# Optimization experiments

Measured on AMD Instinct MI355X. Metric: run time of the kernel, lower is better.

## Reference

```python
import jax, jax.numpy as jnp
import numpy as np

B, T, C = 2, 2048, 2048
N, K, H = 16, 4, 128      # heads, kv heads, head dim
G = N // K                # query groups per kv head
ROPE_THETA = 10000.0
N_LAYERS = 24
SOFTCAP = 50.0


def _sine_table(features, length, max_timescale):
    fraction = jnp.arange(0, features, 2, dtype=jnp.float32) / features
    timescale = max_timescale ** fraction  # min_timescale = 1.0
    sinusoid = jnp.einsum('i,j->ij', jnp.arange(length, dtype=jnp.float32),
                          1.0 / timescale, precision=jax.lax.Precision.HIGHEST)
    sinusoid = jnp.concatenate([sinusoid, sinusoid], axis=-1)  # (length, features)
    return jnp.sin(sinusoid), jnp.cos(sinusoid)


def _rotate_half(x):
    x1, x2 = jnp.split(x, 2, axis=-1)
    return jnp.concatenate([-x2, x1], axis=-1)


def setup_inputs() -> dict:
    key = jax.random.key(0)
    kx, kq, kk, kv, ko = jax.random.split(key, 5)
    init_std = np.sqrt(2.0 / (5.0 * C)).astype(np.float32)
    wang_std = np.float32(2.0 / N_LAYERS / np.sqrt(N * H))
    return {
        'x': jax.random.normal(kx, (B, T, C), dtype=jnp.float32),
        'q_kernel': jax.random.normal(kq, (C, N * H), dtype=jnp.float32) * init_std,
        'k_kernel': jax.random.normal(kk, (C, K * H), dtype=jnp.float32) * init_std,
        'v_kernel': jax.random.normal(kv, (C, K * H), dtype=jnp.float32) * init_std,
        'out_kernel': jax.random.normal(ko, (N * H, C), dtype=jnp.float32) * wang_std,
    }


def reference(x, q_kernel, k_kernel, v_kernel, out_kernel):
    q = jnp.dot(x, q_kernel).reshape(B, T, K, G, H)
    k = jnp.dot(x, k_kernel).reshape(B, T, K, H)
    v = jnp.dot(x, v_kernel).reshape(B, T, K, H)

    # RoPE (note original passes cos into the `sin` slot and vice versa by name,
    # but the computation uses cos with identity part and sin with rotate_half).
    sin, cos = _sine_table(H, T, ROPE_THETA)
    qcos = cos[None, :, None, None, :]  # (1,T,1,1,H)
    qsin = sin[None, :, None, None, :]
    kcos = cos[None, :, None, :]        # (1,T,1,H)
    ksin = sin[None, :, None, :]
    q = q * qcos + _rotate_half(q) * qsin
    k = k * kcos + _rotate_half(k) * ksin

    scale = jax.lax.rsqrt(jnp.float32(H))
    logits = jnp.einsum('btkgh,bskh->bkgts', q * scale, k)  # (B,K,G,T,S)
    logits = jnp.tanh(logits / SOFTCAP) * SOFTCAP
    causal = jnp.tril(jnp.ones((T, T), dtype=jnp.bool_))
    neg = jnp.asarray(-0.7 * jnp.finfo(logits.dtype).max, dtype=logits.dtype)
    logits = jnp.where(causal[None, None, None, :, :], logits, neg)
    probs = jax.nn.softmax(logits.astype(jnp.float32), axis=-1).astype(logits.dtype)
    encoded = jnp.einsum('bkgts,bskh->btkgh', probs, v)
    encoded = encoded.reshape(B, T, N * H)
    return jnp.dot(encoded, out_kernel)
```

## Files before the change

### kernel.cpp

```cpp
#include <hip/hip_runtime.h>
#include <stdint.h>

typedef unsigned short u16;
typedef __bf16 bf16x8 __attribute__((ext_vector_type(8)));
typedef __bf16 bf16x4 __attribute__((ext_vector_type(4)));
typedef float f32x4 __attribute__((ext_vector_type(4)));

#define T_SEQ 2048
#define KVH 4

__device__ __forceinline__ u16 f2b(float f) {
  uint32_t u = __builtin_bit_cast(uint32_t, f);
  u += 0x7FFFu + ((u >> 16) & 1u);
  return (u16)(u >> 16);
}
__device__ __forceinline__ float b2f(u16 h) {
  uint32_t u = ((uint32_t)h) << 16;
  return __builtin_bit_cast(float, u);
}

__device__ __forceinline__ void gload16(const void* g, void* l) {
  __builtin_amdgcn_global_load_lds((const __attribute__((address_space(1))) void*)g,
                                   (__attribute__((address_space(3))) void*)l, 16, 0, 0);
}

__global__ void k_f32_to_bf16(const float* __restrict__ in, u16* __restrict__ out, int n4) {
  int i = blockIdx.x * blockDim.x + threadIdx.x;
  if (i >= n4) return;
  float4 v = reinterpret_cast<const float4*>(in)[i];
  ushort4 o;
  o.x = f2b(v.x); o.y = f2b(v.y); o.z = f2b(v.z); o.w = f2b(v.w);
  reinterpret_cast<ushort4*>(out)[i] = o;
}

__global__ void k_transpose_f32_bf16(const float* __restrict__ in, u16* __restrict__ out,
                                     int R, int Cc) {
  __shared__ float tile[32][33];
  const int c0 = blockIdx.x * 32, r0 = blockIdx.y * 32;
  const int tx = threadIdx.x, ty = threadIdx.y;
  for (int i = ty; i < 32; i += 8) tile[i][tx] = in[(size_t)(r0 + i) * Cc + c0 + tx];
  __syncthreads();
  for (int i = ty; i < 32; i += 8) out[(size_t)(c0 + i) * R + r0 + tx] = f2b(tile[tx][i]);
}

template <int OUT_BF16>
__global__ __launch_bounds__(256, 3) void k_gemm(const u16* __restrict__ A,
                                                 const u16* __restrict__ Bt,
                                                 void* __restrict__ Cp,
                                                 int M, int N, int Kd,
                                                 int lda, int ldb, int ldc) {
  __align__(16) __shared__ u16 As[128 * 32];
  __align__(16) __shared__ u16 Bs[128 * 32];
  const int tid = threadIdx.x;
  const int wid = tid >> 6, lane = tid & 63;
  const int lg = lane >> 4, lm = lane & 15;
  const int bm = blockIdx.x, bn = blockIdx.y;
  const int wr = wid >> 1, wc = wid & 1;

  const int srow = wid * 32 + (lane >> 2);
  const int scol = (lane & 3) * 8;
  const u16* ap0 = A + (size_t)(bm * 128 + srow) * lda + scol;
  const u16* ap1 = ap0 + (size_t)16 * lda;
  const u16* bp0 = Bt + (size_t)(bn * 128 + srow) * ldb + scol;
  const u16* bp1 = bp0 + (size_t)16 * ldb;
  u16* asDst0 = As + wid * 1024;
  u16* asDst1 = As + wid * 1024 + 512;
  u16* bsDst0 = Bs + wid * 1024;
  u16* bsDst1 = Bs + wid * 1024 + 512;

  const f32x4 z4 = {0.f, 0.f, 0.f, 0.f};
  f32x4 acc[4][4];
#pragma unroll
  for (int i = 0; i < 4; ++i)
#pragma unroll
    for (int j = 0; j < 4; ++j) acc[i][j] = z4;

  const int nk = Kd >> 5;
  for (int kb = 0; kb < nk; ++kb) {
    gload16(ap0, asDst0);
    gload16(ap1, asDst1);
    gload16(bp0, bsDst0);
    gload16(bp1, bsDst1);
    ap0 += 32; ap1 += 32; bp0 += 32; bp1 += 32;
    __syncthreads();
    bf16x8 af[4], bfr[4];
#pragma unroll
    for (int i = 0; i < 4; ++i)
      af[i] = *(const bf16x8*)(As + (wr * 64 + i * 16 + lm) * 32 + lg * 8);
#pragma unroll
    for (int j = 0; j < 4; ++j)
      bfr[j] = *(const bf16x8*)(Bs + (wc * 64 + j * 16 + lm) * 32 + lg * 8);
#pragma unroll
    for (int i = 0; i < 4; ++i)
#pragma unroll
      for (int j = 0; j < 4; ++j)
        acc[i][j] = __builtin_amdgcn_mfma_f32_16x16x32_bf16(af[i], bfr[j], acc[i][j], 0, 0, 0);
    __syncthreads();
  }

#pragma unroll
  for (int i = 0; i < 4; ++i) {
    const int row = bm * 128 + wr * 64 + i * 16 + lg * 4;
#pragma unroll
    for (int j = 0; j < 4; ++j) {
      const int col = bn * 128 + wc * 64 + j * 16 + lm;
#pragma unroll
      for (int r = 0; r < 4; ++r) {
        const float v = acc[i][j][r];
        if (OUT_BF16)
          ((u16*)Cp)[(size_t)(row + r) * ldc + col] = __builtin_bit_cast(u16, (__bf16)v);
        else
          ((float*)Cp)[(size_t)(row + r) * ldc + col] = v;
      }
    }
  }
}

__global__ void k_rope_k(const u16* __restrict__ qkv, u16* __restrict__ kbf) {
  const int idx = blockIdx.x * 256 + threadIdx.x;
  const int j = idx & 63;
  const int kh = (idx >> 6) & 3;
  const int m = idx >> 8;
  const int t = m & (T_SEQ - 1);
  const int b = m >> 11;
  const float inv = __expf((float)j * -0.14391157f);
  const float ang = (float)t * inv;
  float s, c;
  __sincosf(ang, &s, &c);
  const u16* row = qkv + (size_t)m * 3072 + 2048 + kh * 128;
  const float x1 = b2f(row[j]), x2 = b2f(row[j + 64]);
  u16* orow = kbf + ((size_t)(b * KVH + kh) * T_SEQ + t) * 128;
  orow[j] = f2b(x1 * c - x2 * s);
  orow[j + 64] = f2b(x2 * c + x1 * s);
}

__global__ void k_v_transpose(const u16* __restrict__ qkv, u16* __restrict__ vt) {
  __shared__ u16 tile[32][33];
  const int t0 = blockIdx.x * 32, h0 = blockIdx.y * 32, bk = blockIdx.z;
  const int b = bk >> 2, kh = bk & 3;
  const int tx = threadIdx.x, ty = threadIdx.y;
  for (int i = ty; i < 32; i += 8)
    tile[i][tx] = qkv[(size_t)(b * T_SEQ + t0 + i) * 3072 + 2560 + kh * 128 + h0 + tx];
  __syncthreads();
  for (int i = ty; i < 32; i += 8)
    vt[(size_t)bk * (128 * T_SEQ) + (size_t)(h0 + i) * T_SEQ + t0 + tx] = tile[tx][i];
}

__global__ __launch_bounds__(256, 2) void k_attn(const u16* __restrict__ qkv,
                                                 const u16* __restrict__ kbf,
                                                 const u16* __restrict__ vt,
                                                 u16* __restrict__ enc) {
  __shared__ __align__(16) u16 smem[36864];
  u16* const Ks0 = smem;
  u16* const Vs0 = smem + 16384;

  const int n = blockIdx.y, b = blockIdx.z;
  const int qt = (b == 0) ? (15 - blockIdx.x) : blockIdx.x;
  const int kh = n >> 2;
  const int tid = threadIdx.x;
  const int wid = tid >> 6;
  const int lane = tid & 63;
  const int lg = lane >> 4;
  const int lm = lane & 15;
  const int q0w = qt * 128 + wid * 32;
  u16* const Pl = smem + 32768 + wid * 1024;

  bf16x8 qfA[4], qfB[4];
  {
    const u16* qa = qkv + (size_t)(b * T_SEQ + q0w + lm) * 3072 + n * 128 + lg * 8;
    const u16* qb_ = qa + 16 * 3072;
    bf16x8 ra[4], rb[4];
#pragma unroll
    for (int c = 0; c < 4; ++c) {
      ra[c] = *(const bf16x8*)(qa + c * 32);
      rb[c] = *(const bf16x8*)(qb_ + c * 32);
    }
    const float scale = 0.08838834764831845f;
    const float tA = (float)(q0w + lm), tB = (float)(q0w + 16 + lm);
#pragma unroll
    for (int c = 0; c < 2; ++c) {
#pragma unroll
      for (int k = 0; k < 8; ++k) {
        const float inv = __expf((float)(c * 32 + lg * 8 + k) * -0.14391157f);
        float sA, cA, sB, cB;
        __sincosf(tA * inv, &sA, &cA);
        __sincosf(tB * inv, &sB, &cB);
        const float a1 = (float)ra[c][k], a2 = (float)ra[c + 2][k];
        const float b1 = (float)rb[c][k], b2 = (float)rb[c + 2][k];
        qfA[c][k]     = (__bf16)((a1 * cA - a2 * sA) * scale);
        qfA[c + 2][k] = (__bf16)((a2 * cA + a1 * sA) * scale);
        qfB[c][k]     = (__bf16)((b1 * cB - b2 * sB) * scale);
        qfB[c + 2][k] = (__bf16)((b2 * cB + b1 * sB) * scale);
      }
    }
  }
  const u16* const kg = kbf + (size_t)(b * KVH + kh) * T_SEQ * 128;
  const u16* const vg = vt + (size_t)(b * KVH + kh) * 128 * T_SEQ;

  const int swz = lm & 7;
  int koff[4], voff[2], poff[4];
#pragma unroll
  for (int c = 0; c < 4; ++c) koff[c] = lm * 128 + (((c * 4 + lg) ^ swz) * 8);
#pragma unroll
  for (int ks = 0; ks < 2; ++ks) voff[ks] = lm * 64 + (((ks * 4 + lg) ^ swz) * 8);
#pragma unroll
  for (int st = 0; st < 4; ++st)
    poff[st] = lm * 64 + (((st * 2 + (lg >> 1)) ^ swz) * 8) + (lg & 1) * 4;

  const f32x4 z4 = {0.f, 0.f, 0.f, 0.f};
  f32x4 accA[8], accB[8];
#pragma unroll
  for (int h = 0; h < 8; ++h) { accA[h] = z4; accB[h] = z4; }
  float lA = 0.f, lB = 0.f;

  const int ntiles = 2 * qt + 2;

  auto STAGE = [&](int buf, int kb2) {
    const int kv2 = kb2 * 64;
    const u16* ksrc = kg + (size_t)kv2 * 128;
    u16* kdst = Ks0 + buf * 8192;
    u16* vdst = Vs0 + buf * 8192;
#pragma unroll
    for (int i = 0; i < 4; ++i) {
      const int g = tid + i * 256;
      const int row = g >> 4, u = g & 15;
      gload16(ksrc + row * 128 + ((u ^ (row & 7)) * 8), kdst + g * 8);
    }
#pragma unroll
    for (int i = 0; i < 4; ++i) {
      const int g = tid + i * 256;
      const int row = g >> 3, u = g & 7;
      gload16(vg + (size_t)row * T_SEQ + kv2 + ((u ^ (row & 7)) * 8), vdst + g * 8);
    }
  };

  auto tile_pc = [&](f32x4* sa, float* p, float& lsum, int tg, bool needMask, int kv) {
#pragma unroll
    for (int st = 0; st < 4; ++st)
#pragma unroll
      for (int r = 0; r < 4; ++r) p[st * 4 + r] = sa[st][r];
#pragma unroll
    for (int i = 0; i < 16; ++i) {
      const float e = __builtin_amdgcn_exp2f(p[i] * 0.05770780163555853f);
      p[i] = __builtin_amdgcn_exp2f(-144.269504088896f * __builtin_amdgcn_rcpf(e + 1.f));
    }
    if (needMask) {
#pragma unroll
      for (int i = 0; i < 16; ++i) {
        const int sg = kv + (i >> 2) * 16 + lg * 4 + (i & 3);
        if (sg > tg) p[i] = 0.f;
      }
    }
#pragma unroll
    for (int i = 0; i < 16; ++i) lsum += p[i];
  };
  auto tile_pw = [&](const float* p) {
#pragma unroll
    for (int st = 0; st < 4; ++st) {
      bf16x4 w4;
#pragma unroll
      for (int r = 0; r < 4; ++r) w4[r] = (__bf16)p[st * 4 + r];
      *(bf16x4*)(Pl + poff[st]) = w4;
    }
  };

  STAGE(0, 0);
  asm volatile("s_waitcnt vmcnt(0)" ::: "memory");
  __syncthreads();

  for (int kb = 0; kb < ntiles; ++kb) {
    const int cur = kb & 1;
    if (kb + 1 < ntiles) STAGE(cur ^ 1, kb + 1);
    const int kv = kb * 64;
    if (kv <= q0w + 31) {
      const u16* KsC = Ks0 + cur * 8192;
      const u16* VsC = Vs0 + cur * 8192;

      f32x4 saA[4] = {z4, z4, z4, z4};
      f32x4 saB[4] = {z4, z4, z4, z4};
      __builtin_amdgcn_s_setprio(1);
#pragma unroll
      for (int st = 0; st < 4; ++st) {
#pragma unroll
        for (int c = 0; c < 4; ++c) {
          const bf16x8 kf = *(const bf16x8*)(KsC + st * 2048 + koff[c]);
          saA[st] = __builtin_amdgcn_mfma_f32_16x16x32_bf16(kf, qfA[c], saA[st], 0, 0, 0);
          saB[st] = __builtin_amdgcn_mfma_f32_16x16x32_bf16(kf, qfB[c], saB[st], 0, 0, 0);
        }
      }
      __builtin_amdgcn_s_setprio(0);

      float pA[16], pB[16];
      tile_pc(saA, pA, lA, q0w + lm, kv + 63 > q0w, kv);
      tile_pw(pA);
      tile_pc(saB, pB, lB, q0w + 16 + lm, kv + 63 > q0w + 16, kv);
      asm volatile("s_waitcnt lgkmcnt(0)" ::: "memory");
      bf16x8 pfA[2], pfB[2];
#pragma unroll
      for (int ks = 0; ks < 2; ++ks) pfA[ks] = *(const bf16x8*)(Pl + voff[ks]);
      tile_pw(pB);
      asm volatile("s_waitcnt lgkmcnt(0)" ::: "memory");
#pragma unroll
      for (int ks = 0; ks < 2; ++ks) pfB[ks] = *(const bf16x8*)(Pl + voff[ks]);

      __builtin_amdgcn_s_setprio(1);
#pragma unroll
      for (int h = 0; h < 8; ++h) {
#pragma unroll
        for (int ks = 0; ks < 2; ++ks) {
          const bf16x8 vf = *(const bf16x8*)(VsC + h * 1024 + voff[ks]);
          accA[h] = __builtin_amdgcn_mfma_f32_16x16x32_bf16(pfA[ks], vf, accA[h], 0, 0, 0);
          accB[h] = __builtin_amdgcn_mfma_f32_16x16x32_bf16(pfB[ks], vf, accB[h], 0, 0, 0);
        }
      }
      __builtin_amdgcn_s_setprio(0);
    }
    asm volatile("s_waitcnt vmcnt(0)" ::: "memory");
    __syncthreads();
  }

  lA += __shfl_xor(lA, 16); lA += __shfl_xor(lA, 32);
  lB += __shfl_xor(lB, 16); lB += __shfl_xor(lB, 32);
  float liA[4], liB[4];
#pragma unroll
  for (int r = 0; r < 4; ++r) {
    liA[r] = 1.f / __shfl(lA, lg * 4 + r);
    liB[r] = 1.f / __shfl(lB, lg * 4 + r);
  }
#pragma unroll
  for (int h = 0; h < 8; ++h) {
#pragma unroll
    for (int r = 0; r < 4; ++r) {
      const size_t colo = n * 128 + h * 16 + lm;
      enc[(size_t)(b * T_SEQ + q0w + lg * 4 + r) * 2048 + colo] =
          __builtin_bit_cast(u16, (__bf16)(accA[h][r] * liA[r]));
      enc[(size_t)(b * T_SEQ + q0w + 16 + lg * 4 + r) * 2048 + colo] =
          __builtin_bit_cast(u16, (__bf16)(accB[h][r] * liB[r]));
    }
  }
}

extern "C" void kernel_launch(void* const* d_in, const int* in_sizes, int n_in,
                              void* d_out, int out_size, void* d_ws, size_t ws_size,
                              hipStream_t stream) {
  const float* x  = (const float*)d_in[0];
  const float* wq = (const float*)d_in[1];
  const float* wk = (const float*)d_in[2];
  const float* wv = (const float*)d_in[3];
  const float* wo = (const float*)d_in[4];

  char* ws = (char*)d_ws;
  u16* x_bf  = (u16*)(ws);
  u16* wqkvt = (u16*)(ws + 16777216);
  u16* wot   = (u16*)(ws + 29360128);
  u16* qkv   = (u16*)(ws + 37748736);
  u16* enc   = (u16*)(ws + 62914560);
  u16* k_bf  = (u16*)(ws + 79691776);
  u16* vt    = (u16*)(ws + 83886080);
  if (ws_size < 88080384) return;
  (void)in_sizes; (void)n_in; (void)out_size;

  k_f32_to_bf16<<<dim3(8192), dim3(256), 0, stream>>>(x, x_bf, 8388608 / 4);
  k_transpose_f32_bf16<<<dim3(64, 64), dim3(32, 8), 0, stream>>>(wq, wqkvt, 2048, 2048);
  k_transpose_f32_bf16<<<dim3(16, 64), dim3(32, 8), 0, stream>>>(wk, wqkvt + 2048 * 2048, 2048, 512);
  k_transpose_f32_bf16<<<dim3(16, 64), dim3(32, 8), 0, stream>>>(wv, wqkvt + 2560 * 2048, 2048, 512);
  k_transpose_f32_bf16<<<dim3(64, 64), dim3(32, 8), 0, stream>>>(wo, wot, 2048, 2048);
  k_gemm<1><<<dim3(32, 24), dim3(256), 0, stream>>>(x_bf, wqkvt, qkv,
                                                    4096, 3072, 2048, 2048, 2048, 3072);
  k_rope_k<<<dim3(4096), dim3(256), 0, stream>>>(qkv, k_bf);
  k_v_transpose<<<dim3(64, 4, 8), dim3(32, 8), 0, stream>>>(qkv, vt);
  k_attn<<<dim3(16, 16, 2), dim3(256), 0, stream>>>(qkv, k_bf, vt, enc);
  k_gemm<0><<<dim3(32, 16), dim3(256), 0, stream>>>(enc, wot, d_out,
                                                    4096, 2048, 2048, 2048, 2048, 2048);
}
```

Before: 208.8 us.

## Split attention KV range across two warp halves with 4-stage prefetch pipeline

The attention block grows from 256 to 512 threads. Two groups of four waves each process a different 32-key half of every 64-key tile for the same query rows. K/V staging becomes a 4-deep ring buffer with vmcnt-based waits instead of a full drain per tile, and the two halves' partial outputs and row sums are combined through shared memory at the end. This doubles the waves available to hide latency and overlaps loads further ahead, at the cost of double LDS use (one block per CU), a final reduction pass, and narrower MFMA work per wave.

After: 227.2 us. +8.8%, slower.

```diff
diff --git a/kernel.cpp b/kernel.cpp
--- a/kernel.cpp
+++ b/kernel.cpp
@@ -146,24 +146,24 @@
     vt[(size_t)bk * (128 * T_SEQ) + (size_t)(h0 + i) * T_SEQ + t0 + tx] = tile[tx][i];
 }
 
-__global__ __launch_bounds__(256, 2) void k_attn(const u16* __restrict__ qkv,
+__global__ __launch_bounds__(512, 1) void k_attn(const u16* __restrict__ qkv,
                                                  const u16* __restrict__ kbf,
                                                  const u16* __restrict__ vt,
                                                  u16* __restrict__ enc) {
-  __shared__ __align__(16) u16 smem[36864];
-  u16* const Ks0 = smem;
-  u16* const Vs0 = smem + 16384;
+  __shared__ __align__(16) u16 smem[73728];
 
   const int n = blockIdx.y, b = blockIdx.z;
   const int qt = (b == 0) ? (15 - blockIdx.x) : blockIdx.x;
   const int kh = n >> 2;
   const int tid = threadIdx.x;
   const int wid = tid >> 6;
+  const int half = wid >> 2;
+  const int wq = wid & 3;
   const int lane = tid & 63;
   const int lg = lane >> 4;
   const int lm = lane & 15;
-  const int q0w = qt * 128 + wid * 32;
-  u16* const Pl = smem + 32768 + wid * 1024;
+  const int q0w = qt * 128 + wq * 32;
+  u16* const Pl = smem + 65536 + wid * 1024;
 
   bf16x8 qfA[4], qfB[4];
   {
@@ -197,15 +197,14 @@
   const u16* const kg = kbf + (size_t)(b * KVH + kh) * T_SEQ * 128;
   const u16* const vg = vt + (size_t)(b * KVH + kh) * 128 * T_SEQ;
 
-  const int swz = lm & 7;
-  int koff[4], voff[2], poff[4];
-#pragma unroll
-  for (int c = 0; c < 4; ++c) koff[c] = lm * 128 + (((c * 4 + lg) ^ swz) * 8);
-#pragma unroll
-  for (int ks = 0; ks < 2; ++ks) voff[ks] = lm * 64 + (((ks * 4 + lg) ^ swz) * 8);
-#pragma unroll
-  for (int st = 0; st < 4; ++st)
-    poff[st] = lm * 64 + (((st * 2 + (lg >> 1)) ^ swz) * 8) + (lg & 1) * 4;
+  int koff[4];
+#pragma unroll
+  for (int c = 0; c < 4; ++c) koff[c] = lm * 128 + (((c * 4 + lg) ^ (lm & 7)) * 8);
+  const int voffb = lm * 32 + ((lg ^ (lm & 3)) * 8);
+  int poff[2];
+#pragma unroll
+  for (int st = 0; st < 2; ++st)
+    poff[st] = lm * 32 + (((st * 2 + (lg >> 1)) ^ (lm & 3)) * 8) + (lg & 1) * 4;
 
   const f32x4 z4 = {0.f, 0.f, 0.f, 0.f};
   f32x4 accA[8], accB[8];
@@ -215,48 +214,46 @@
 
   const int ntiles = 2 * qt + 2;
 
-  auto STAGE = [&](int buf, int kb2) {
-    const int kv2 = kb2 * 64;
-    const u16* ksrc = kg + (size_t)kv2 * 128;
-    u16* kdst = Ks0 + buf * 8192;
-    u16* vdst = Vs0 + buf * 8192;
-#pragma unroll
-    for (int i = 0; i < 4; ++i) {
-      const int g = tid + i * 256;
-      const int row = g >> 4, u = g & 15;
-      gload16(ksrc + row * 128 + ((u ^ (row & 7)) * 8), kdst + g * 8);
-    }
-#pragma unroll
-    for (int i = 0; i < 4; ++i) {
-      const int g = tid + i * 256;
-      const int row = g >> 3, u = g & 7;
-      gload16(vg + (size_t)row * T_SEQ + kv2 + ((u ^ (row & 7)) * 8), vdst + g * 8);
+  auto STAGE = [&](int buf, int j2) {
+#pragma unroll
+    for (int hh = 0; hh < 2; ++hh) {
+      const int kv2 = j2 * 64 + hh * 32;
+      {
+        const int row = tid >> 4, u = tid & 15;
+        gload16(kg + (size_t)(kv2 + row) * 128 + ((u ^ (row & 7)) * 8),
+                smem + (buf * 2 + hh) * 4096 + tid * 8);
+      }
+      {
+        const int row = tid >> 2, u = tid & 3;
+        gload16(vg + (size_t)row * T_SEQ + kv2 + ((u ^ (row & 3)) * 8),
+                smem + 32768 + (buf * 2 + hh) * 4096 + tid * 8);
+      }
     }
   };
 
-  auto tile_pc = [&](f32x4* sa, float* p, float& lsum, int tg, bool needMask, int kv) {
-#pragma unroll
-    for (int st = 0; st < 4; ++st)
+  auto tile_pc = [&](f32x4* sa, float* p, float& lsum, int tg, bool needMask, int kvh) {
+#pragma unroll
+    for (int st = 0; st < 2; ++st)
 #pragma unroll
       for (int r = 0; r < 4; ++r) p[st * 4 + r] = sa[st][r];
 #pragma unroll
-    for (int i = 0; i < 16; ++i) {
+    for (int i = 0; i < 8; ++i) {
       const float e = __builtin_amdgcn_exp2f(p[i] * 0.05770780163555853f);
       p[i] = __builtin_amdgcn_exp2f(-144.269504088896f * __builtin_amdgcn_rcpf(e + 1.f));
     }
     if (needMask) {
 #pragma unroll
-      for (int i = 0; i < 16; ++i) {
-        const int sg = kv + (i >> 2) * 16 + lg * 4 + (i & 3);
+      for (int i = 0; i < 8; ++i) {
+        const int sg = kvh + (i >> 2) * 16 + lg * 4 + (i & 3);
         if (sg > tg) p[i] = 0.f;
       }
     }
 #pragma unroll
-    for (int i = 0; i < 16; ++i) lsum += p[i];
+    for (int i = 0; i < 8; ++i) lsum += p[i];
   };
   auto tile_pw = [&](const float* p) {
 #pragma unroll
-    for (int st = 0; st < 4; ++st) {
+    for (int st = 0; st < 2; ++st) {
       bf16x4 w4;
 #pragma unroll
       for (int r = 0; r < 4; ++r) w4[r] = (__bf16)p[st * 4 + r];
@@ -264,78 +261,113 @@
     }
   };
 
+  auto COMPUTE = [&](int j) {
+    const int kvh = j * 64 + half * 32;
+    if (kvh > q0w + 31) return;
+    const u16* KsC = smem + ((j & 3) * 2 + half) * 4096;
+    const u16* VsC = smem + 32768 + ((j & 3) * 2 + half) * 4096;
+
+    f32x4 saA[2] = {z4, z4}, saB[2] = {z4, z4};
+    __builtin_amdgcn_s_setprio(1);
+#pragma unroll
+    for (int st = 0; st < 2; ++st) {
+#pragma unroll
+      for (int c = 0; c < 4; ++c) {
+        const bf16x8 kf = *(const bf16x8*)(KsC + st * 2048 + koff[c]);
+        saA[st] = __builtin_amdgcn_mfma_f32_16x16x32_bf16(kf, qfA[c], saA[st], 0, 0, 0);
+        saB[st] = __builtin_amdgcn_mfma_f32_16x16x32_bf16(kf, qfB[c], saB[st], 0, 0, 0);
+      }
+    }
+    __builtin_amdgcn_s_setprio(0);
+
+    float pA[8], pB[8];
+    tile_pc(saA, pA, lA, q0w + lm, kvh + 31 > q0w, kvh);
+    tile_pw(pA);
+    tile_pc(saB, pB, lB, q0w + 16 + lm, kvh + 31 > q0w + 16, kvh);
+    asm volatile("s_waitcnt lgkmcnt(0)" ::: "memory");
+    const bf16x8 pfA = *(const bf16x8*)(Pl + voffb);
+    tile_pw(pB);
+    asm volatile("s_waitcnt lgkmcnt(0)" ::: "memory");
+    const bf16x8 pfB = *(const bf16x8*)(Pl + voffb);
+
+    __builtin_amdgcn_s_setprio(1);
+#pragma unroll
+    for (int h = 0; h < 8; ++h) {
+      const bf16x8 vf = *(const bf16x8*)(VsC + h * 512 + voffb);
+      accA[h] = __builtin_amdgcn_mfma_f32_16x16x32_bf16(pfA, vf, accA[h], 0, 0, 0);
+      accB[h] = __builtin_amdgcn_mfma_f32_16x16x32_bf16(pfB, vf, accB[h], 0, 0, 0);
+    }
+    __builtin_amdgcn_s_setprio(0);
+  };
+
   STAGE(0, 0);
-  asm volatile("s_waitcnt vmcnt(0)" ::: "memory");
+  STAGE(1, 1);
+  for (int j = 0; j < ntiles - 2; ++j) {
+    STAGE((j + 2) & 3, j + 2);
+    asm volatile("s_waitcnt vmcnt(8)" ::: "memory");
+    __builtin_amdgcn_s_barrier();
+    __builtin_amdgcn_sched_barrier(0);
+    COMPUTE(j);
+  }
+  {
+    asm volatile("s_waitcnt vmcnt(4)" ::: "memory");
+    __builtin_amdgcn_s_barrier();
+    __builtin_amdgcn_sched_barrier(0);
+    COMPUTE(ntiles - 2);
+  }
+  {
+    asm volatile("s_waitcnt vmcnt(0)" ::: "memory");
+    __builtin_amdgcn_s_barrier();
+    __builtin_amdgcn_sched_barrier(0);
+    COMPUTE(ntiles - 1);
+  }
+
   __syncthreads();
-
-  for (int kb = 0; kb < ntiles; ++kb) {
-    const int cur = kb & 1;
-    if (kb + 1 < ntiles) STAGE(cur ^ 1, kb + 1);
-    const int kv = kb * 64;
-    if (kv <= q0w + 31) {
-      const u16* KsC = Ks0 + cur * 8192;
-      const u16* VsC = Vs0 + cur * 8192;
-
-      f32x4 saA[4] = {z4, z4, z4, z4};
-      f32x4 saB[4] = {z4, z4, z4, z4};
-      __builtin_amdgcn_s_setprio(1);
-#pragma unroll
-      for (int st = 0; st < 4; ++st) {
-#pragma unroll
-        for (int c = 0; c < 4; ++c) {
-          const bf16x8 kf = *(const bf16x8*)(KsC + st * 2048 + koff[c]);
-          saA[st] = __builtin_amdgcn_mfma_f32_16x16x32_bf16(kf, qfA[c], saA[st], 0, 0, 0);
-          saB[st] = __builtin_amdgcn_mfma_f32_16x16x32_bf16(kf, qfB[c], saB[st], 0, 0, 0);
-        }
-      }
-      __builtin_amdgcn_s_setprio(0);
-
-      float pA[16], pB[16];
-      tile_pc(saA, pA, lA, q0w + lm, kv + 63 > q0w, kv);
-      tile_pw(pA);
-      tile_pc(saB, pB, lB, q0w + 16 + lm, kv + 63 > q0w + 16, kv);
-      asm volatile("s_waitcnt lgkmcnt(0)" ::: "memory");
-      bf16x8 pfA[2], pfB[2];
-#pragma unroll
-      for (int ks = 0; ks < 2; ++ks) pfA[ks] = *(const bf16x8*)(Pl + voff[ks]);
-      tile_pw(pB);
-      asm volatile("s_waitcnt lgkmcnt(0)" ::: "memory");
-#pragma unroll
-      for (int ks = 0; ks < 2; ++ks) pfB[ks] = *(const bf16x8*)(Pl + voff[ks]);
-
-      __builtin_amdgcn_s_setprio(1);
-#pragma unroll
-      for (int h = 0; h < 8; ++h) {
-#pragma unroll
-        for (int ks = 0; ks < 2; ++ks) {
-          const bf16x8 vf = *(const bf16x8*)(VsC + h * 1024 + voff[ks]);
-          accA[h] = __builtin_amdgcn_mfma_f32_16x16x32_bf16(pfA[ks], vf, accA[h], 0, 0, 0);
-          accB[h] = __builtin_amdgcn_mfma_f32_16x16x32_bf16(pfB[ks], vf, accB[h], 0, 0, 0);
-        }
-      }
-      __builtin_amdgcn_s_setprio(0);
-    }
-    asm volatile("s_waitcnt vmcnt(0)" ::: "memory");
-    __syncthreads();
-  }
-
-  lA += __shfl_xor(lA, 16); lA += __shfl_xor(lA, 32);
-  lB += __shfl_xor(lB, 16); lB += __shfl_xor(lB, 32);
-  float liA[4], liB[4];
-#pragma unroll
-  for (int r = 0; r < 4; ++r) {
-    liA[r] = 1.f / __shfl(lA, lg * 4 + r);
-    liB[r] = 1.f / __shfl(lB, lg * 4 + r);
-  }
-#pragma unroll
-  for (int h = 0; h < 8; ++h) {
+  float* const scrO = (float*)smem;
+  float* const scrL = (float*)smem + 16384;
+  if (half == 1) {
+    float* w = scrO + wq * 4096 + lane;
+#pragma unroll
+    for (int h = 0; h < 8; ++h)
+#pragma unroll
+      for (int r = 0; r < 4; ++r) {
+        w[(h * 4 + r) * 64] = accA[h][r];
+        w[(32 + h * 4 + r) * 64] = accB[h][r];
+      }
+    scrL[wq * 128 + lane * 2] = lA;
+    scrL[wq * 128 + lane * 2 + 1] = lB;
+  }
+  __syncthreads();
+  if (half == 0) {
+    const float* w = scrO + wq * 4096 + lane;
+#pragma unroll
+    for (int h = 0; h < 8; ++h)
+#pragma unroll
+      for (int r = 0; r < 4; ++r) {
+        accA[h][r] += w[(h * 4 + r) * 64];
+        accB[h][r] += w[(32 + h * 4 + r) * 64];
+      }
+    lA += scrL[wq * 128 + lane * 2];
+    lB += scrL[wq * 128 + lane * 2 + 1];
+
+    lA += __shfl_xor(lA, 16); lA += __shfl_xor(lA, 32);
+    lB += __shfl_xor(lB, 16); lB += __shfl_xor(lB, 32);
+    float liA[4], liB[4];
 #pragma unroll
     for (int r = 0; r < 4; ++r) {
-      const size_t colo = n * 128 + h * 16 + lm;
-      enc[(size_t)(b * T_SEQ + q0w + lg * 4 + r) * 2048 + colo] =
-          __builtin_bit_cast(u16, (__bf16)(accA[h][r] * liA[r]));
-      enc[(size_t)(b * T_SEQ + q0w + 16 + lg * 4 + r) * 2048 + colo] =
-          __builtin_bit_cast(u16, (__bf16)(accB[h][r] * liB[r]));
+      liA[r] = 1.f / __shfl(lA, lg * 4 + r);
+      liB[r] = 1.f / __shfl(lB, lg * 4 + r);
+    }
+#pragma unroll
+    for (int h = 0; h < 8; ++h) {
+#pragma unroll
+      for (int r = 0; r < 4; ++r) {
+        const size_t colo = n * 128 + h * 16 + lm;
+        enc[(size_t)(b * T_SEQ + q0w + lg * 4 + r) * 2048 + colo] =
+            __builtin_bit_cast(u16, (__bf16)(accA[h][r] * liA[r]));
+        enc[(size_t)(b * T_SEQ + q0w + 16 + lg * 4 + r) * 2048 + colo] =
+            __builtin_bit_cast(u16, (__bf16)(accB[h][r] * liB[r]));
+      }
     }
   }
 }
@@ -369,7 +401,7 @@
                                                     4096, 3072, 2048, 2048, 2048, 3072);
   k_rope_k<<<dim3(4096), dim3(256), 0, stream>>>(qkv, k_bf);
   k_v_transpose<<<dim3(64, 4, 8), dim3(32, 8), 0, stream>>>(qkv, vt);
-  k_attn<<<dim3(16, 16, 2), dim3(256), 0, stream>>>(qkv, k_bf, vt, enc);
+  k_attn<<<dim3(16, 16, 2), dim3(512), 0, stream>>>(qkv, k_bf, vt, enc);
   k_gemm<0><<<dim3(32, 16), dim3(256), 0, stream>>>(enc, wot, d_out,
                                                     4096, 2048, 2048, 2048, 2048, 2048);
 }
```
